# Optimization experiments

Hardware: AMD Instinct MI355X
Metric: run time of the kernel (lower is better)

The kernel has to match this reference:

```python
import jax, jax.numpy as jnp
import numpy as np


def setup_inputs() -> dict:
    key = jax.random.key(0)
    k1, k2, k3, k4 = jax.random.split(key, 4)
    N, S, F, UNITS = 50000, 32, 128, 128
    x = jax.random.normal(k1, (N, F), dtype=jnp.float32)
    neigh_x = jax.random.normal(k2, (N, S, F), dtype=jnp.float32)
    kernel_self = jax.random.normal(k3, (F, UNITS), dtype=jnp.float32) * 0.05
    kernel_neigh = jax.random.normal(k4, (F, UNITS), dtype=jnp.float32) * 0.05
    bias = jnp.zeros((2 * UNITS,), dtype=jnp.float32)
    return {"x": x, "neigh_x": neigh_x, "kernel_self": kernel_self,
            "kernel_neigh": kernel_neigh, "bias": bias}


def reference(x, neigh_x, kernel_self, kernel_neigh, bias):
    # neigh_x: [N, S, F]. Original transposes to [N, F, S] and applies
    # tf.raw_ops.NthElement with n = S//2 + S%2 (n-th smallest, 0-indexed)
    # along the last (neighbor) axis. Equivalent: sort along neighbor axis
    # of the untransposed tensor and take index n.
    S = neigh_x.shape[1]
    n = S // 2 + S % 2
    med = jnp.sort(neigh_x, axis=1)[:, n, :]  # [N, F]
    out = jnp.concatenate([x @ kernel_self, med @ kernel_neigh], axis=1)  # [N, 2*units] (concat=True)
    out = out + bias
    return jax.nn.relu(out)
```

## Files before the change

kernel.cpp:

```cpp
#include <hip/hip_runtime.h>

namespace {

typedef float f32x2 __attribute__((ext_vector_type(2)));
typedef float f32x4 __attribute__((ext_vector_type(4)));

constexpr int S   = 32;
constexpr int F   = 128;
constexpr int BR  = 32;
constexpr int TPB = 256;

struct CEPair { int a, b; };

constexpr int batcher_count16() {
  int n = 16, cnt = 0;
  for (int p = 1; p < n; p <<= 1)
    for (int k = p; k >= 1; k >>= 1)
      for (int j = k % p; j + k < n; j += 2 * k)
        for (int i = 0; i < k && i + j + k < n; ++i)
          if ((i + j) / (2 * p) == (i + j + k) / (2 * p))
            ++cnt;
  return cnt;
}
constexpr int NCE = batcher_count16();

struct Net16 { CEPair ce[NCE]; };

constexpr Net16 make_net16() {
  Net16 net{};
  int n = 16, c = 0;
  for (int p = 1; p < n; p <<= 1)
    for (int k = p; k >= 1; k >>= 1)
      for (int j = k % p; j + k < n; j += 2 * k)
        for (int i = 0; i < k && i + j + k < n; ++i)
          if ((i + j) / (2 * p) == (i + j + k) / (2 * p))
            net.ce[c++] = CEPair{i + j, i + j + k};
  return net;
}
constexpr Net16 NET16 = make_net16();

__device__ __forceinline__ f32x2 min2(f32x2 a, f32x2 b) {
  f32x2 r; r.x = fminf(a.x, b.x); r.y = fminf(a.y, b.y); return r;
}
__device__ __forceinline__ f32x2 max2(f32x2 a, f32x2 b) {
  f32x2 r; r.x = fmaxf(a.x, b.x); r.y = fmaxf(a.y, b.y); return r;
}

template<int T>
__device__ __forceinline__ void sort16(f32x2 (&v)[16]) {
  if constexpr (T < NCE) {
    constexpr int a = NET16.ce[T].a;
    constexpr int b = NET16.ce[T].b;
    f32x2 x = v[a], y = v[b];
    v[a] = min2(x, y);
    v[b] = max2(x, y);
    sort16<T + 1>(v);
  }
}

__global__ __launch_bounds__(TPB, 4) void fused_median_gemm(
    const float* __restrict__ x,
    const float* __restrict__ neigh,
    const float* __restrict__ Ks,
    const float* __restrict__ Kn,
    const float* __restrict__ bias,
    float* __restrict__ out,
    int N)
{
    __shared__ __align__(16) float xs[4][8][F];
    __shared__ __align__(16) float ms[4][8][F];

    const int tid  = threadIdx.x;
    const int wv   = tid >> 6;
    const int lane = tid & 63;
    const int row0 = blockIdx.x * BR + wv * 8;

#pragma unroll 1
    for (int r = 0; r < 8; ++r) {
        int row = row0 + r;
        if (row > N - 1) row = N - 1;
        const f32x2* base =
            (const f32x2*)(neigh + (size_t)row * (S * F)) + lane;

        const f32x2 xv =
            *((const f32x2*)(x + (size_t)row * F) + lane);

        f32x2 A[16], B[16];
#pragma unroll
        for (int s = 0; s < 16; ++s)
            A[s] = __builtin_nontemporal_load(base + (size_t)s * 64);
#pragma unroll
        for (int s = 0; s < 16; ++s)
            B[s] = __builtin_nontemporal_load(base + (size_t)(16 + s) * 64);

        sort16<0>(A);
        sort16<0>(B);

        f32x2 c[16];
#pragma unroll
        for (int q = 0; q < 16; ++q) c[q] = max2(A[q], B[15 - q]);
#pragma unroll
        for (int st = 8; st >= 1; st >>= 1)
#pragma unroll
            for (int q = 0; q < st; ++q) c[q] = min2(c[q], c[q + st]);

        ((f32x2*)&ms[wv][r][0])[lane] = c[0];
        ((f32x2*)&xs[wv][r][0])[lane] = xv;
    }

    __threadfence_block();

    const bool self_half = (lane < 32);
    const float* __restrict__ W = self_half ? Ks : Kn;
    const int wcol = (lane * 4) & 127;
    const float* lin = self_half ? &xs[wv][0][0] : &ms[wv][0][0];

    f32x4 acc[8];
#pragma unroll
    for (int r = 0; r < 8; ++r) acc[r] = f32x4{0.f, 0.f, 0.f, 0.f};

#pragma unroll 4
    for (int k4 = 0; k4 < 32; ++k4) {
        f32x4 wv4[4];
#pragma unroll
        for (int dk = 0; dk < 4; ++dk)
            wv4[dk] = *(const f32x4*)&W[(k4 * 4 + dk) * 128 + wcol];

        f32x4 xr[8];
#pragma unroll
        for (int r = 0; r < 8; ++r)
            xr[r] = *(const f32x4*)&lin[r * F + k4 * 4];

#pragma unroll
        for (int r = 0; r < 8; ++r) {
#pragma unroll
            for (int dk = 0; dk < 4; ++dk) {
                const float s = xr[r][dk];
                acc[r].x = fmaf(s, wv4[dk].x, acc[r].x);
                acc[r].y = fmaf(s, wv4[dk].y, acc[r].y);
                acc[r].z = fmaf(s, wv4[dk].z, acc[r].z);
                acc[r].w = fmaf(s, wv4[dk].w, acc[r].w);
            }
        }
    }

    const f32x4 bv = *(const f32x4*)&bias[lane * 4];
#pragma unroll
    for (int r = 0; r < 8; ++r) {
        int row = row0 + r;
        if (row > N - 1) row = N - 1;
        f32x4 o;
        o.x = fmaxf(acc[r].x + bv.x, 0.f);
        o.y = fmaxf(acc[r].y + bv.y, 0.f);
        o.z = fmaxf(acc[r].z + bv.z, 0.f);
        o.w = fmaxf(acc[r].w + bv.w, 0.f);
        __builtin_nontemporal_store(o, (f32x4*)&out[(size_t)row * 256 + lane * 4]);
    }
}

}

extern "C" void kernel_launch(void* const* d_in, const int* in_sizes, int n_in,
                              void* d_out, int out_size, void* d_ws, size_t ws_size,
                              hipStream_t stream) {
    const float* x     = (const float*)d_in[0];
    const float* neigh = (const float*)d_in[1];
    const float* Ks    = (const float*)d_in[2];
    const float* Kn    = (const float*)d_in[3];
    const float* bias  = (const float*)d_in[4];
    float* out = (float*)d_out;

    const int N = in_sizes[0] / F;
    const int grid = (N + BR - 1) / BR;
    hipLaunchKernelGGL(fused_median_gemm, dim3(grid), dim3(TPB), 0, stream,
                       x, neigh, Ks, Kn, bias, out, N);
}
```

Baseline: 198.7 us.

## Double-buffer neighbor row loads to overlap global fetch with median sort

Restructures the per-wave row loop into a software pipeline that issues the loads for the next row into a second register set while the current row is sorted and reduced to its median. This is meant to hide global memory latency behind the sorting-network ALU work within each wave. It doubles register use for the staging arrays, so the occupancy hint drops from 4 to 3 blocks per CU. The block fence is replaced with an explicit LDS waitcnt.

```diff
diff --git a/kernel.cpp b/kernel.cpp
--- a/kernel.cpp
+++ b/kernel.cpp
@@ -58,7 +58,41 @@
   }
 }
 
-__global__ __launch_bounds__(TPB, 4) void fused_median_gemm(
+__device__ __forceinline__ void issue_row(const float* __restrict__ neigh,
+                                          const float* __restrict__ x,
+                                          int row, int lane,
+                                          f32x2 (&A)[16], f32x2 (&B)[16],
+                                          f32x2& xv)
+{
+    const f32x2* nb = (const f32x2*)(neigh + (size_t)row * (S * F)) + lane;
+#pragma unroll
+    for (int s = 0; s < 16; ++s)
+        A[s] = __builtin_nontemporal_load(nb + (size_t)s * 64);
+#pragma unroll
+    for (int s = 0; s < 16; ++s)
+        B[s] = __builtin_nontemporal_load(nb + (size_t)(s + 16) * 64);
+    xv = *((const f32x2*)(x + (size_t)row * F) + lane);
+}
+
+__device__ __forceinline__ void select_store(f32x2 (&A)[16], f32x2 (&B)[16],
+                                             f32x2 xv,
+                                             float* __restrict__ msrow,
+                                             float* __restrict__ xsrow,
+                                             int lane)
+{
+    sort16<0>(A);
+    sort16<0>(B);
+#pragma unroll
+    for (int q = 0; q < 16; ++q) A[q] = max2(A[q], B[15 - q]);
+#pragma unroll
+    for (int st = 8; st >= 1; st >>= 1)
+#pragma unroll
+        for (int q = 0; q < st; ++q) A[q] = min2(A[q], A[q + st]);
+    ((f32x2*)msrow)[lane] = A[0];
+    ((f32x2*)xsrow)[lane] = xv;
+}
+
+__global__ __launch_bounds__(TPB, 3) void fused_median_gemm(
     const float* __restrict__ x,
     const float* __restrict__ neigh,
     const float* __restrict__ Ks,
@@ -75,40 +109,25 @@
     const int lane = tid & 63;
     const int row0 = blockIdx.x * BR + wv * 8;
 
-#pragma unroll 1
-    for (int r = 0; r < 8; ++r) {
-        int row = row0 + r;
-        if (row > N - 1) row = N - 1;
-        const f32x2* base =
-            (const f32x2*)(neigh + (size_t)row * (S * F)) + lane;
+    const int rmax = N - 1;
+    auto rw = [&](int rl) { int r = row0 + rl; return r > rmax ? rmax : r; };
 
-        const f32x2 xv =
-            *((const f32x2*)(x + (size_t)row * F) + lane);
+    {
+        f32x2 A0[16], B0[16], A1[16], B1[16];
+        f32x2 x0, x1;
 
-        f32x2 A[16], B[16];
+        issue_row(neigh, x, rw(0), lane, A0, B0, x0);
 #pragma unroll
-        for (int s = 0; s < 16; ++s)
-            A[s] = __builtin_nontemporal_load(base + (size_t)s * 64);
-#pragma unroll
-        for (int s = 0; s < 16; ++s)
-            B[s] = __builtin_nontemporal_load(base + (size_t)(16 + s) * 64);
-
-        sort16<0>(A);
-        sort16<0>(B);
-
-        f32x2 c[16];
-#pragma unroll
-        for (int q = 0; q < 16; ++q) c[q] = max2(A[q], B[15 - q]);
-#pragma unroll
-        for (int st = 8; st >= 1; st >>= 1)
-#pragma unroll
-            for (int q = 0; q < st; ++q) c[q] = min2(c[q], c[q + st]);
-
-        ((f32x2*)&ms[wv][r][0])[lane] = c[0];
-        ((f32x2*)&xs[wv][r][0])[lane] = xv;
+        for (int p = 0; p < 4; ++p) {
+            issue_row(neigh, x, rw(2 * p + 1), lane, A1, B1, x1);
+            select_store(A0, B0, x0, &ms[wv][2 * p][0], &xs[wv][2 * p][0], lane);
+            if (p < 3)
+                issue_row(neigh, x, rw(2 * p + 2), lane, A0, B0, x0);
+            select_store(A1, B1, x1, &ms[wv][2 * p + 1][0], &xs[wv][2 * p + 1][0], lane);
+        }
     }
 
-    __threadfence_block();
+    asm volatile("s_waitcnt lgkmcnt(0)" ::: "memory");
 
     const bool self_half = (lane < 32);
     const float* __restrict__ W = self_half ? Ks : Kn;
@@ -147,8 +166,7 @@
     const f32x4 bv = *(const f32x4*)&bias[lane * 4];
 #pragma unroll
     for (int r = 0; r < 8; ++r) {
-        int row = row0 + r;
-        if (row > N - 1) row = N - 1;
+        const int row = rw(r);
         f32x4 o;
         o.x = fmaxf(acc[r].x + bv.x, 0.f);
         o.y = fmaxf(acc[r].y + bv.y, 0.f);
```

Result: faster. 183.6 us (-7.6%).

## Software-pipeline neighbor loads by half-rows with scalar per-lane elements

Applied to the files above, without the earlier changes.

Each row's neighbor data is split into two 64-column halves processed with scalar floats, and the load for the next half is issued before sorting the current one, double-buffering registers so global latency overlaps the sorting network. The vectorized nontemporal f32x2 loads become scalar regular loads. The block fence is replaced by an explicit lgkmcnt wait. This risks narrower memory transactions, extra register pressure from two buffers, and losing the nontemporal cache hint.

```diff
diff --git a/kernel.cpp b/kernel.cpp
--- a/kernel.cpp
+++ b/kernel.cpp
@@ -2,7 +2,6 @@
 
 namespace {
 
-typedef float f32x2 __attribute__((ext_vector_type(2)));
 typedef float f32x4 __attribute__((ext_vector_type(4)));
 
 constexpr int S   = 32;
@@ -39,23 +38,48 @@
 }
 constexpr Net16 NET16 = make_net16();
 
-__device__ __forceinline__ f32x2 min2(f32x2 a, f32x2 b) {
-  f32x2 r; r.x = fminf(a.x, b.x); r.y = fminf(a.y, b.y); return r;
-}
-__device__ __forceinline__ f32x2 max2(f32x2 a, f32x2 b) {
-  f32x2 r; r.x = fmaxf(a.x, b.x); r.y = fmaxf(a.y, b.y); return r;
-}
-
 template<int T>
-__device__ __forceinline__ void sort16(f32x2 (&v)[16]) {
+__device__ __forceinline__ void sort16(float (&v)[16]) {
   if constexpr (T < NCE) {
     constexpr int a = NET16.ce[T].a;
     constexpr int b = NET16.ce[T].b;
-    f32x2 x = v[a], y = v[b];
-    v[a] = min2(x, y);
-    v[b] = max2(x, y);
+    float x = v[a], y = v[b];
+    v[a] = fminf(x, y);
+    v[b] = fmaxf(x, y);
     sort16<T + 1>(v);
   }
+}
+
+__device__ __forceinline__ void issue_half(const float* __restrict__ neigh,
+                                           const float* __restrict__ x,
+                                           int row, int h, int lane,
+                                           float (&A)[16], float (&B)[16],
+                                           float& xv)
+{
+    const float* nb = neigh + (size_t)row * (S * F) + h * 64 + lane;
+#pragma unroll
+    for (int s = 0; s < 16; ++s) A[s] = nb[s * F];
+#pragma unroll
+    for (int s = 0; s < 16; ++s) B[s] = nb[(s + 16) * F];
+    xv = x[(size_t)row * F + h * 64 + lane];
+}
+
+__device__ __forceinline__ void select_store(float (&A)[16], float (&B)[16],
+                                             float xv,
+                                             float* __restrict__ msrow,
+                                             float* __restrict__ xsrow,
+                                             int h, int lane)
+{
+    sort16<0>(A);
+    sort16<0>(B);
+#pragma unroll
+    for (int q = 0; q < 16; ++q) A[q] = fmaxf(A[q], B[15 - q]);
+#pragma unroll
+    for (int st = 8; st >= 1; st >>= 1)
+#pragma unroll
+        for (int q = 0; q < st; ++q) A[q] = fminf(A[q], A[q + st]);
+    msrow[h * 64 + lane] = A[0];
+    xsrow[h * 64 + lane] = xv;
 }
 
 __global__ __launch_bounds__(TPB, 4) void fused_median_gemm(
@@ -75,40 +99,28 @@
     const int lane = tid & 63;
     const int row0 = blockIdx.x * BR + wv * 8;
 
+    const int rmax = N - 1;
+    auto rw = [&](int hp) { int r = row0 + (hp >> 1); return r > rmax ? rmax : r; };
+
+    {
+        float A0[16], B0[16], A1[16], B1[16];
+        float x0, x1;
+
+        issue_half(neigh, x, rw(0), 0, lane, A0, B0, x0);
 #pragma unroll 1
-    for (int r = 0; r < 8; ++r) {
-        int row = row0 + r;
-        if (row > N - 1) row = N - 1;
-        const f32x2* base =
-            (const f32x2*)(neigh + (size_t)row * (S * F)) + lane;
-
-        const f32x2 xv =
-            *((const f32x2*)(x + (size_t)row * F) + lane);
-
-        f32x2 A[16], B[16];
-#pragma unroll
-        for (int s = 0; s < 16; ++s)
-            A[s] = __builtin_nontemporal_load(base + (size_t)s * 64);
-#pragma unroll
-        for (int s = 0; s < 16; ++s)
-            B[s] = __builtin_nontemporal_load(base + (size_t)(16 + s) * 64);
-
-        sort16<0>(A);
-        sort16<0>(B);
-
-        f32x2 c[16];
-#pragma unroll
-        for (int q = 0; q < 16; ++q) c[q] = max2(A[q], B[15 - q]);
-#pragma unroll
-        for (int st = 8; st >= 1; st >>= 1)
-#pragma unroll
-            for (int q = 0; q < st; ++q) c[q] = min2(c[q], c[q + st]);
-
-        ((f32x2*)&ms[wv][r][0])[lane] = c[0];
-        ((f32x2*)&xs[wv][r][0])[lane] = xv;
+        for (int p = 0; p < 8; ++p) {
+            const int h0 = (2 * p) & 1, h1 = (2 * p + 1) & 1;
+            issue_half(neigh, x, rw(2 * p + 1), 1, lane, A1, B1, x1);
+            select_store(A0, B0, x0, &ms[wv][(2 * p) >> 1][0],
+                         &xs[wv][(2 * p) >> 1][0], h0, lane);
+            if (p < 7)
+                issue_half(neigh, x, rw(2 * p + 2), 0, lane, A0, B0, x0);
+            select_store(A1, B1, x1, &ms[wv][(2 * p + 1) >> 1][0],
+                         &xs[wv][(2 * p + 1) >> 1][0], h1, lane);
+        }
     }
 
-    __threadfence_block();
+    asm volatile("s_waitcnt lgkmcnt(0)" ::: "memory");
 
     const bool self_half = (lane < 32);
     const float* __restrict__ W = self_half ? Ks : Kn;
@@ -148,7 +160,7 @@
 #pragma unroll
     for (int r = 0; r < 8; ++r) {
         int row = row0 + r;
-        if (row > N - 1) row = N - 1;
+        if (row > rmax) row = rmax;
         f32x4 o;
         o.x = fmaxf(acc[r].x + bv.x, 0.f);
         o.y = fmaxf(acc[r].y + bv.y, 0.f);
```

Result: slower. 218.3 us (+9.9%).
